# Kernel optimization log

Hardware: AMD Instinct MI355X
Metric: run time of the kernel (lower is better)

Reference implementation:

```python
import jax, jax.numpy as jnp
import numpy as np

WINDOW_SIZE = 11
CHANNEL = 3
SIGMA = 1.5
C1 = 0.01 ** 2
C2 = 0.03 ** 2


def _create_window(window_size: int, channel: int) -> jnp.ndarray:
    coords = jnp.arange(window_size, dtype=jnp.float32) - window_size // 2
    g = jnp.exp(-coords ** 2 / (2 * SIGMA ** 2))
    g = g / g.sum()
    w2d = jnp.outer(g, g)  # [K, K]
    # depthwise conv kernel, OIHW with O=channel, I=1
    return jnp.broadcast_to(w2d, (channel, 1, window_size, window_size))


def _depthwise_conv(x, window):
    pad = WINDOW_SIZE // 2
    return jax.lax.conv_general_dilated(
        x, window,
        window_strides=(1, 1),
        padding=[(pad, pad), (pad, pad)],
        dimension_numbers=("NCHW", "OIHW", "NCHW"),
        feature_group_count=x.shape[1],
    )


def setup_inputs() -> dict:
    key = jax.random.key(0)
    k1, k2 = jax.random.split(key)
    pred = jax.random.uniform(k1, (16, 3, 512, 512), dtype=jnp.float32)
    target = jax.random.uniform(k2, (16, 3, 512, 512), dtype=jnp.float32)
    window = _create_window(WINDOW_SIZE, CHANNEL)
    return {"pred": pred, "target": target, "window": window}


def reference(pred, target, window):
    mu1 = _depthwise_conv(pred, window)
    mu2 = _depthwise_conv(target, window)
    mu1_sq = mu1 * mu1
    mu2_sq = mu2 * mu2
    mu1_mu2 = mu1 * mu2
    sigma1_sq = _depthwise_conv(pred * pred, window) - mu1_sq
    sigma2_sq = _depthwise_conv(target * target, window) - mu2_sq
    sigma12 = _depthwise_conv(pred * target, window) - mu1_mu2
    ssim_map = ((2 * mu1_mu2 + C1) * (2 * sigma12 + C2)) / (
        (mu1_sq + mu2_sq + C1) * (sigma1_sq + sigma2_sq + C2)
    )
    return 1.0 - ssim_map.mean()
```

## Files before the change

kernel.cpp:

```cpp
#include <hip/hip_runtime.h>

#define IMG_H 512
#define IMG_W 512
#define IMG_N (IMG_H * IMG_W)
#define NPLANES 48
#define TILE 64
#define XS 88
#define SSIM_C1 0.0001f
#define SSIM_C2 0.0009f

typedef _Float16 f16x2 __attribute__((ext_vector_type(2)));
typedef _Float16 f16x4 __attribute__((ext_vector_type(4)));
typedef _Float16 f16x8 __attribute__((ext_vector_type(8)));
typedef float    f32x4 __attribute__((ext_vector_type(4)));

__device__ __forceinline__ unsigned pk2(float a, float b) {
    return __builtin_bit_cast(unsigned,
        __builtin_amdgcn_cvt_pkrtz(a, b));
}
__device__ __forceinline__ f16x2 pk2h(float a, float b) {
    return __builtin_bit_cast(f16x2, __builtin_amdgcn_cvt_pkrtz(a, b));
}

__global__ __launch_bounds__(256) void ssim_mfma_kernel(
    const float* __restrict__ pred, const float* __restrict__ target,
    const float* __restrict__ window, float* __restrict__ partial)
{
    __shared__ unsigned short Xp[80 * XS];
    __shared__ unsigned short Xt[80 * XS];
    __shared__ unsigned short gfS[16];
    __shared__ float wsum[4];

    const int tid  = threadIdx.x;
    const int w    = tid >> 6;
    const int lane = tid & 63;
    const int n15  = lane & 15;
    const int quad = lane >> 4;

    if (tid < 16) {
        float gv = 0.f;
        if (tid < 11) {
            float s = 0.f;
            #pragma unroll
            for (int j = 0; j < 11; ++j) s += window[tid * 11 + j];
            gv = s;
        }
        const _Float16 hg = (_Float16)gv;
        gfS[tid] = __builtin_bit_cast(unsigned short, hg);
    }

    const int plane  = blockIdx.z;
    const int base_r = blockIdx.y * TILE;
    const int base_c = blockIdx.x * TILE;
    const float* pp = pred   + (size_t)plane * IMG_N;
    const float* tp = target + (size_t)plane * IMG_N;

    #pragma unroll
    for (int i = 0; i < 7; ++i) {
        const unsigned fi = (unsigned)tid + 256u * i;
        if (fi < 1600u) {
            const unsigned ri = fi / 20u, q = fi - 20u * ri;
            const int gr = base_r - 8 + (int)ri;
            const int gc = base_c - 8 + 4 * (int)q;
            const bool ok = ((unsigned)gr < (unsigned)IMG_H) &&
                            ((unsigned)gc < (unsigned)IMG_W);
            const float4 z4 = make_float4(0.f, 0.f, 0.f, 0.f);
            float4 p4 = ok ? *(const float4*)(pp + gr * IMG_W + gc) : z4;
            float4 t4 = ok ? *(const float4*)(tp + gr * IMG_W + gc) : z4;
            const int off = (int)ri * XS + 4 * (int)q;
            *(uint2*)&Xp[off] = make_uint2(pk2(p4.x, p4.y), pk2(p4.z, p4.w));
            *(uint2*)&Xt[off] = make_uint2(pk2(t4.x, t4.y), pk2(t4.z, t4.w));
        }
    }
    __syncthreads();

    uint4 wu;
    {
        unsigned wd[4];
        #pragma unroll
        for (int d = 0; d < 4; ++d) {
            const int t0 = 8 * quad + 2 * d - n15 - 3;
            const unsigned lo = gfS[((unsigned)t0       <= 10u) ? t0       : 11];
            const unsigned hi = gfS[((unsigned)(t0 + 1) <= 10u) ? (t0 + 1) : 11];
            wd[d] = lo | (hi << 16);
        }
        wu = make_uint4(wd[0], wd[1], wd[2], wd[3]);
    }
    const f16x8 wfrag = __builtin_bit_cast(f16x8, wu);

    f16x4 w0frag, w1frag;
    {
        unsigned a[2], b[2];
        #pragma unroll
        for (int d = 0; d < 2; ++d) {
            const int k0 = 4 * quad + 2 * d;
            const int a0 = k0 - n15 - 3,  a1 = a0 + 1;
            const int b0 = k0 - n15 + 13, b1 = b0 + 1;
            a[d] = gfS[((unsigned)a0 <= 10u) ? a0 : 11] |
                   ((unsigned)gfS[((unsigned)a1 <= 10u) ? a1 : 11] << 16);
            b[d] = gfS[((unsigned)b0 <= 10u) ? b0 : 11] |
                   ((unsigned)gfS[((unsigned)b1 <= 10u) ? b1 : 11] << 16);
        }
        w0frag = __builtin_bit_cast(f16x4, make_uint2(a[0], a[1]));
        w1frag = __builtin_bit_cast(f16x4, make_uint2(b[0], b[1]));
    }
    const f32x4 zero4 = {0.f, 0.f, 0.f, 0.f};

    auto h_tile = [&](int h, f16x4 (&P)[5]) {
        const int xoff = (16 * h + n15) * XS + 16 * w + 8 * quad;
        const f16x8 pu = *(const f16x8*)&Xp[xoff];
        const f16x8 tu = *(const f16x8*)&Xt[xoff];
        #pragma unroll
        for (int ch = 0; ch < 5; ++ch) {
            f16x8 au;
            if      (ch == 0) au = pu;
            else if (ch == 1) au = tu;
            else if (ch == 2) au = pu * pu;
            else if (ch == 3) au = tu * tu;
            else              au = pu * tu;
            const f32x4 hd = __builtin_amdgcn_mfma_f32_16x16x32_f16(
                au, wfrag, zero4, 0, 0, 0);
            const f16x2 l  = pk2h(hd[0], hd[1]);
            const f16x2 hh = pk2h(hd[2], hd[3]);
            P[ch] = f16x4{l.x, l.y, hh.x, hh.y};
        }
    };

    f16x4 Pprev[5], Pcur[5];
    h_tile(0, Pprev);

    float acc = 0.f;
    #pragma unroll
    for (int rt = 0; rt < 4; ++rt) {
        h_tile(rt + 1, Pcur);
        f32x4 s[5];
        #pragma unroll
        for (int ch = 0; ch < 5; ++ch) {
            const f32x4 t = __builtin_amdgcn_mfma_f32_16x16x16f16(
                w0frag, Pprev[ch], zero4, 0, 0, 0);
            s[ch] = __builtin_amdgcn_mfma_f32_16x16x16f16(
                w1frag, Pcur[ch], t, 0, 0, 0);
        }
        #pragma unroll
        for (int r = 0; r < 4; ++r) {
            const float mu1 = s[0][r], mu2 = s[1][r];
            const float e11 = s[2][r], e22 = s[3][r], e12 = s[4][r];
            const float mu1_sq = mu1 * mu1, mu2_sq = mu2 * mu2;
            const float mu1_mu2 = mu1 * mu2;
            const float s1  = e11 - mu1_sq;
            const float s2  = e22 - mu2_sq;
            const float s12 = e12 - mu1_mu2;
            const float num = (2.f * mu1_mu2 + SSIM_C1) * (2.f * s12 + SSIM_C2);
            const float den = (mu1_sq + mu2_sq + SSIM_C1) * (s1 + s2 + SSIM_C2);
            acc += num * __builtin_amdgcn_rcpf(den);
        }
        #pragma unroll
        for (int ch = 0; ch < 5; ++ch) Pprev[ch] = Pcur[ch];
    }

    #pragma unroll
    for (int off = 32; off > 0; off >>= 1)
        acc += __shfl_down(acc, off, 64);
    if (lane == 0) wsum[w] = acc;
    __syncthreads();
    if (tid == 0) {
        const int bid = blockIdx.x + gridDim.x * (blockIdx.y + gridDim.y * blockIdx.z);
        partial[bid] = wsum[0] + wsum[1] + wsum[2] + wsum[3];
    }
}

__global__ __launch_bounds__(256) void ssim_reduce_kernel(
    const float* __restrict__ partial, float* __restrict__ out)
{
    const int tid = threadIdx.x;
    float s = 0.f;
    #pragma unroll
    for (int k = 0; k < 12; ++k) s += partial[tid + 256 * k];
    double acc = (double)s;
    #pragma unroll
    for (int off = 32; off > 0; off >>= 1)
        acc += __shfl_down(acc, off, 64);
    __shared__ double wsumd[4];
    const int lane = tid & 63, wid = tid >> 6;
    if (lane == 0) wsumd[wid] = acc;
    __syncthreads();
    if (tid == 0) {
        const double total = wsumd[0] + wsumd[1] + wsumd[2] + wsumd[3];
        const double N = (double)NPLANES * IMG_H * IMG_W;
        out[0] = (float)(1.0 - total / N);
    }
}

extern "C" void kernel_launch(void* const* d_in, const int* in_sizes, int n_in,
                              void* d_out, int out_size, void* d_ws, size_t ws_size,
                              hipStream_t stream)
{
    const float* pred   = (const float*)d_in[0];
    const float* target = (const float*)d_in[1];
    const float* window = (const float*)d_in[2];
    float* out = (float*)d_out;
    float* partial = (float*)d_ws;

    dim3 grid(IMG_W / TILE, IMG_H / TILE, NPLANES);
    ssim_mfma_kernel<<<grid, 256, 0, stream>>>(pred, target, window, partial);
    ssim_reduce_kernel<<<1, 256, 0, stream>>>(partial, out);
}
```

Before: 146.6 us.

## Batch all global tile loads before LDS stores, specialize interior blocks

Input staging now issues all seven float4 loads per input before any conversion or LDS store, so more memory requests are in flight at once. Interior blocks use a template path with no bounds checks, while edge blocks clamp addresses and zero out-of-range values afterwards. The LDS row stride shrinks from 88 to 80 halves, the LDS arrays are 16-byte aligned, and launch bounds request 6 blocks per CU. The trade-off is higher register pressure from the buffered loads, and the new stride may change the LDS bank-conflict pattern for the MFMA fragment reads.

```diff
diff --git a/kernel.cpp b/kernel.cpp
--- a/kernel.cpp
+++ b/kernel.cpp
@@ -5,7 +5,7 @@
 #define IMG_N (IMG_H * IMG_W)
 #define NPLANES 48
 #define TILE 64
-#define XS 88
+#define XS 80
 #define SSIM_C1 0.0001f
 #define SSIM_C2 0.0009f
 
@@ -22,12 +22,55 @@
     return __builtin_bit_cast(f16x2, __builtin_amdgcn_cvt_pkrtz(a, b));
 }
 
-__global__ __launch_bounds__(256) void ssim_mfma_kernel(
+template <bool CHECK>
+__device__ __forceinline__ void stage_inputs(
+    const float* __restrict__ pp, const float* __restrict__ tp,
+    unsigned short* Xp, unsigned short* Xt,
+    const int tid, const int base_r, const int base_c)
+{
+    float4   pb[7], tb[7];
+    unsigned offv[7];
+    bool     okv[7];
+    #pragma unroll
+    for (int i = 0; i < 7; ++i) {
+        unsigned fi = (unsigned)tid + 256u * i;
+        if (i == 6) fi = (fi < 1600u) ? fi : 0u;
+        const unsigned ri = fi / 20u;
+        const unsigned q  = fi - 20u * ri;
+        int gr = base_r - 8 + (int)ri;
+        int gc = base_c - 8 + 4 * (int)q;
+        bool ok = true;
+        if (CHECK) {
+            ok = ((unsigned)gr < (unsigned)IMG_H) && ((unsigned)gc < (unsigned)IMG_W);
+            gr = min(max(gr, 0), IMG_H - 1);
+            gc = min(max(gc, 0), IMG_W - 4);
+        }
+        const int idx = gr * IMG_W + gc;
+        pb[i]   = *(const float4*)(pp + idx);
+        tb[i]   = *(const float4*)(tp + idx);
+        okv[i]  = ok;
+        offv[i] = ri * XS + 4u * q;
+    }
+    #pragma unroll
+    for (int i = 0; i < 7; ++i) {
+        float4 p4 = pb[i], t4 = tb[i];
+        if (CHECK && !okv[i]) {
+            p4 = make_float4(0.f, 0.f, 0.f, 0.f);
+            t4 = make_float4(0.f, 0.f, 0.f, 0.f);
+        }
+        if (i < 6 || tid < 64) {
+            *(uint2*)&Xp[offv[i]] = make_uint2(pk2(p4.x, p4.y), pk2(p4.z, p4.w));
+            *(uint2*)&Xt[offv[i]] = make_uint2(pk2(t4.x, t4.y), pk2(t4.z, t4.w));
+        }
+    }
+}
+
+__global__ __launch_bounds__(256, 6) void ssim_mfma_kernel(
     const float* __restrict__ pred, const float* __restrict__ target,
     const float* __restrict__ window, float* __restrict__ partial)
 {
-    __shared__ unsigned short Xp[80 * XS];
-    __shared__ unsigned short Xt[80 * XS];
+    __shared__ __attribute__((aligned(16))) unsigned short Xp[80 * XS];
+    __shared__ __attribute__((aligned(16))) unsigned short Xt[80 * XS];
     __shared__ unsigned short gfS[16];
     __shared__ float wsum[4];
 
@@ -55,23 +98,10 @@
     const float* pp = pred   + (size_t)plane * IMG_N;
     const float* tp = target + (size_t)plane * IMG_N;
 
-    #pragma unroll
-    for (int i = 0; i < 7; ++i) {
-        const unsigned fi = (unsigned)tid + 256u * i;
-        if (fi < 1600u) {
-            const unsigned ri = fi / 20u, q = fi - 20u * ri;
-            const int gr = base_r - 8 + (int)ri;
-            const int gc = base_c - 8 + 4 * (int)q;
-            const bool ok = ((unsigned)gr < (unsigned)IMG_H) &&
-                            ((unsigned)gc < (unsigned)IMG_W);
-            const float4 z4 = make_float4(0.f, 0.f, 0.f, 0.f);
-            float4 p4 = ok ? *(const float4*)(pp + gr * IMG_W + gc) : z4;
-            float4 t4 = ok ? *(const float4*)(tp + gr * IMG_W + gc) : z4;
-            const int off = (int)ri * XS + 4 * (int)q;
-            *(uint2*)&Xp[off] = make_uint2(pk2(p4.x, p4.y), pk2(p4.z, p4.w));
-            *(uint2*)&Xt[off] = make_uint2(pk2(t4.x, t4.y), pk2(t4.z, t4.w));
-        }
-    }
+    const bool interior = (blockIdx.x > 0) && (blockIdx.x < gridDim.x - 1) &&
+                          (blockIdx.y > 0) && (blockIdx.y < gridDim.y - 1);
+    if (interior) stage_inputs<false>(pp, tp, Xp, Xt, tid, base_r, base_c);
+    else          stage_inputs<true >(pp, tp, Xp, Xt, tid, base_r, base_c);
     __syncthreads();
 
     uint4 wu;
```

Result: faster. 128.8 us (-12.1%).

## Load input tiles directly from global into MFMA fragments, dropping LDS staging

Applied to the files above, without the earlier changes.

Removes the shared-memory staging of the 80x80 halo tile. Each lane now loads its 8-wide row segments straight from global memory and packs them to fp16 for the horizontal MFMA. Interior blocks use an unchecked fast path, and border blocks clamp the address and zero out-of-range data. This drops a barrier and the LDS traffic and allows higher occupancy (launch bounds 256,6), but each halo row is now loaded redundantly from global memory or cache by several waves and row tiles.

```diff
diff --git a/kernel.cpp b/kernel.cpp
--- a/kernel.cpp
+++ b/kernel.cpp
@@ -5,7 +5,6 @@
 #define IMG_N (IMG_H * IMG_W)
 #define NPLANES 48
 #define TILE 64
-#define XS 88
 #define SSIM_C1 0.0001f
 #define SSIM_C2 0.0009f
 
@@ -14,102 +13,49 @@
 typedef _Float16 f16x8 __attribute__((ext_vector_type(8)));
 typedef float    f32x4 __attribute__((ext_vector_type(4)));
 
-__device__ __forceinline__ unsigned pk2(float a, float b) {
-    return __builtin_bit_cast(unsigned,
-        __builtin_amdgcn_cvt_pkrtz(a, b));
-}
 __device__ __forceinline__ f16x2 pk2h(float a, float b) {
     return __builtin_bit_cast(f16x2, __builtin_amdgcn_cvt_pkrtz(a, b));
 }
-
-__global__ __launch_bounds__(256) void ssim_mfma_kernel(
-    const float* __restrict__ pred, const float* __restrict__ target,
-    const float* __restrict__ window, float* __restrict__ partial)
-{
-    __shared__ unsigned short Xp[80 * XS];
-    __shared__ unsigned short Xt[80 * XS];
-    __shared__ unsigned short gfS[16];
-    __shared__ float wsum[4];
-
-    const int tid  = threadIdx.x;
-    const int w    = tid >> 6;
-    const int lane = tid & 63;
-    const int n15  = lane & 15;
-    const int quad = lane >> 4;
-
-    if (tid < 16) {
-        float gv = 0.f;
-        if (tid < 11) {
-            float s = 0.f;
-            #pragma unroll
-            for (int j = 0; j < 11; ++j) s += window[tid * 11 + j];
-            gv = s;
-        }
-        const _Float16 hg = (_Float16)gv;
-        gfS[tid] = __builtin_bit_cast(unsigned short, hg);
-    }
-
-    const int plane  = blockIdx.z;
-    const int base_r = blockIdx.y * TILE;
-    const int base_c = blockIdx.x * TILE;
-    const float* pp = pred   + (size_t)plane * IMG_N;
-    const float* tp = target + (size_t)plane * IMG_N;
-
-    #pragma unroll
-    for (int i = 0; i < 7; ++i) {
-        const unsigned fi = (unsigned)tid + 256u * i;
-        if (fi < 1600u) {
-            const unsigned ri = fi / 20u, q = fi - 20u * ri;
-            const int gr = base_r - 8 + (int)ri;
-            const int gc = base_c - 8 + 4 * (int)q;
+__device__ __forceinline__ f16x8 pk8(float4 a, float4 b) {
+    const f16x2 r0 = pk2h(a.x, a.y), r1 = pk2h(a.z, a.w);
+    const f16x2 r2 = pk2h(b.x, b.y), r3 = pk2h(b.z, b.w);
+    return f16x8{r0.x, r0.y, r1.x, r1.y, r2.x, r2.y, r3.x, r3.y};
+}
+
+template <bool CHECK>
+__device__ __forceinline__ float ssim_body(
+    const float* __restrict__ pp, const float* __restrict__ tp,
+    const int base_r, const int base_c, const int cw,
+    const int n15, const int quad,
+    const f16x8 wfrag, const f16x4 w0frag, const f16x4 w1frag)
+{
+    const f32x4 zero4 = {0.f, 0.f, 0.f, 0.f};
+    const int gc = base_c + 16 * cw - 8 + 8 * quad;
+
+    auto h_tile = [&](int h, f16x4 (&P)[5]) {
+        const int gr = base_r - 8 + 16 * h + n15;
+        float4 p0, p1, t0, t1;
+        if (CHECK) {
             const bool ok = ((unsigned)gr < (unsigned)IMG_H) &&
                             ((unsigned)gc < (unsigned)IMG_W);
-            const float4 z4 = make_float4(0.f, 0.f, 0.f, 0.f);
-            float4 p4 = ok ? *(const float4*)(pp + gr * IMG_W + gc) : z4;
-            float4 t4 = ok ? *(const float4*)(tp + gr * IMG_W + gc) : z4;
-            const int off = (int)ri * XS + 4 * (int)q;
-            *(uint2*)&Xp[off] = make_uint2(pk2(p4.x, p4.y), pk2(p4.z, p4.w));
-            *(uint2*)&Xt[off] = make_uint2(pk2(t4.x, t4.y), pk2(t4.z, t4.w));
-        }
-    }
-    __syncthreads();
-
-    uint4 wu;
-    {
-        unsigned wd[4];
-        #pragma unroll
-        for (int d = 0; d < 4; ++d) {
-            const int t0 = 8 * quad + 2 * d - n15 - 3;
-            const unsigned lo = gfS[((unsigned)t0       <= 10u) ? t0       : 11];
-            const unsigned hi = gfS[((unsigned)(t0 + 1) <= 10u) ? (t0 + 1) : 11];
-            wd[d] = lo | (hi << 16);
-        }
-        wu = make_uint4(wd[0], wd[1], wd[2], wd[3]);
-    }
-    const f16x8 wfrag = __builtin_bit_cast(f16x8, wu);
-
-    f16x4 w0frag, w1frag;
-    {
-        unsigned a[2], b[2];
-        #pragma unroll
-        for (int d = 0; d < 2; ++d) {
-            const int k0 = 4 * quad + 2 * d;
-            const int a0 = k0 - n15 - 3,  a1 = a0 + 1;
-            const int b0 = k0 - n15 + 13, b1 = b0 + 1;
-            a[d] = gfS[((unsigned)a0 <= 10u) ? a0 : 11] |
-                   ((unsigned)gfS[((unsigned)a1 <= 10u) ? a1 : 11] << 16);
-            b[d] = gfS[((unsigned)b0 <= 10u) ? b0 : 11] |
-                   ((unsigned)gfS[((unsigned)b1 <= 10u) ? b1 : 11] << 16);
-        }
-        w0frag = __builtin_bit_cast(f16x4, make_uint2(a[0], a[1]));
-        w1frag = __builtin_bit_cast(f16x4, make_uint2(b[0], b[1]));
-    }
-    const f32x4 zero4 = {0.f, 0.f, 0.f, 0.f};
-
-    auto h_tile = [&](int h, f16x4 (&P)[5]) {
-        const int xoff = (16 * h + n15) * XS + 16 * w + 8 * quad;
-        const f16x8 pu = *(const f16x8*)&Xp[xoff];
-        const f16x8 tu = *(const f16x8*)&Xt[xoff];
+            const int grc = min(max(gr, 0), IMG_H - 1);
+            const int gcc = min(max(gc, 0), IMG_W - 8);
+            const float* pr = pp + grc * IMG_W + gcc;
+            const float* tr = tp + grc * IMG_W + gcc;
+            p0 = *(const float4*)(pr);     p1 = *(const float4*)(pr + 4);
+            t0 = *(const float4*)(tr);     t1 = *(const float4*)(tr + 4);
+            if (!ok) {
+                const float4 z = make_float4(0.f, 0.f, 0.f, 0.f);
+                p0 = z; p1 = z; t0 = z; t1 = z;
+            }
+        } else {
+            const float* pr = pp + gr * IMG_W + gc;
+            const float* tr = tp + gr * IMG_W + gc;
+            p0 = *(const float4*)(pr);     p1 = *(const float4*)(pr + 4);
+            t0 = *(const float4*)(tr);     t1 = *(const float4*)(tr + 4);
+        }
+        const f16x8 pu = pk8(p0, p1);
+        const f16x8 tu = pk8(t0, t1);
         #pragma unroll
         for (int ch = 0; ch < 5; ++ch) {
             f16x8 au;
@@ -157,11 +103,86 @@
         #pragma unroll
         for (int ch = 0; ch < 5; ++ch) Pprev[ch] = Pcur[ch];
     }
+    return acc;
+}
+
+__global__ __launch_bounds__(256, 6) void ssim_mfma_kernel(
+    const float* __restrict__ pred, const float* __restrict__ target,
+    const float* __restrict__ window, float* __restrict__ partial)
+{
+    __shared__ unsigned short gfS[16];
+    __shared__ float wsum[4];
+
+    const int tid  = threadIdx.x;
+    const int cw   = tid >> 6;
+    const int lane = tid & 63;
+    const int n15  = lane & 15;
+    const int quad = lane >> 4;
+
+    if (tid < 16) {
+        float gv = 0.f;
+        if (tid < 11) {
+            float s = 0.f;
+            #pragma unroll
+            for (int j = 0; j < 11; ++j) s += window[tid * 11 + j];
+            gv = s;
+        }
+        const _Float16 hg = (_Float16)gv;
+        gfS[tid] = __builtin_bit_cast(unsigned short, hg);
+    }
+    __syncthreads();
+
+    uint4 wu;
+    {
+        unsigned wd[4];
+        #pragma unroll
+        for (int d = 0; d < 4; ++d) {
+            const int t0 = 8 * quad + 2 * d - n15 - 3;
+            const unsigned lo = gfS[((unsigned)t0       <= 10u) ? t0       : 11];
+            const unsigned hi = gfS[((unsigned)(t0 + 1) <= 10u) ? (t0 + 1) : 11];
+            wd[d] = lo | (hi << 16);
+        }
+        wu = make_uint4(wd[0], wd[1], wd[2], wd[3]);
+    }
+    const f16x8 wfrag = __builtin_bit_cast(f16x8, wu);
+
+    f16x4 w0frag, w1frag;
+    {
+        unsigned a[2], b[2];
+        #pragma unroll
+        for (int d = 0; d < 2; ++d) {
+            const int k0 = 4 * quad + 2 * d;
+            const int a0 = k0 - n15 - 3,  a1 = a0 + 1;
+            const int b0 = k0 - n15 + 13, b1 = b0 + 1;
+            a[d] = gfS[((unsigned)a0 <= 10u) ? a0 : 11] |
+                   ((unsigned)gfS[((unsigned)a1 <= 10u) ? a1 : 11] << 16);
+            b[d] = gfS[((unsigned)b0 <= 10u) ? b0 : 11] |
+                   ((unsigned)gfS[((unsigned)b1 <= 10u) ? b1 : 11] << 16);
+        }
+        w0frag = __builtin_bit_cast(f16x4, make_uint2(a[0], a[1]));
+        w1frag = __builtin_bit_cast(f16x4, make_uint2(b[0], b[1]));
+    }
+
+    const int plane  = blockIdx.z;
+    const int base_r = blockIdx.y * TILE;
+    const int base_c = blockIdx.x * TILE;
+    const float* pp = pred   + (size_t)plane * IMG_N;
+    const float* tp = target + (size_t)plane * IMG_N;
+
+    const bool interior = (blockIdx.x > 0) && (blockIdx.x < gridDim.x - 1) &&
+                          (blockIdx.y > 0) && (blockIdx.y < gridDim.y - 1);
+    float acc;
+    if (interior)
+        acc = ssim_body<false>(pp, tp, base_r, base_c, cw, n15, quad,
+                               wfrag, w0frag, w1frag);
+    else
+        acc = ssim_body<true >(pp, tp, base_r, base_c, cw, n15, quad,
+                               wfrag, w0frag, w1frag);
 
     #pragma unroll
     for (int off = 32; off > 0; off >>= 1)
         acc += __shfl_down(acc, off, 64);
-    if (lane == 0) wsum[w] = acc;
+    if (lane == 0) wsum[cw] = acc;
     __syncthreads();
     if (tid == 0) {
         const int bid = blockIdx.x + gridDim.x * (blockIdx.y + gridDim.y * blockIdx.z);
```

Measured after the change: 159.7 us. 1.09x slower.
